# Kernel tuning notes

Measured on AMD Instinct MI355X. Metric: run time of the kernel, lower is better.

Reference implementation:

```python
import jax, jax.numpy as jnp
import numpy as np

EPS_NORM = 1e-12   # F.normalize eps
EPS_DIST = 1e-4    # sqrt stabilizer from original code
EPSILON = 1e-8     # log stabilizer (forward default arg)


def setup_inputs() -> dict:
    key = jax.random.key(0)
    thought_vectors = jax.random.normal(key, (4, 2048, 1024), dtype=jnp.float32)
    return {"thought_vectors": thought_vectors}


def reference(thought_vectors):
    # NOTE: original code casts to fp32 then discards it by re-reshaping the
    # raw input; inputs here are already fp32 so the math is identical.
    D = thought_vectors.shape[-1]
    x = thought_vectors.reshape(-1, D)                          # [N, D]
    norm = jnp.linalg.norm(x, axis=-1, keepdims=True)
    x = x / jnp.maximum(norm, EPS_NORM)                         # L2 normalize
    N = x.shape[0]
    sim = jnp.minimum(jnp.einsum('nd,md->nm', x, x), 1.0)       # [N, N], clamp max=1
    dists = jnp.sqrt(2.0 - 2.0 * sim + EPS_DIST)                # chordal distance
    dists = jnp.where(jnp.eye(N, dtype=bool), jnp.inf, dists)   # mask self
    min_dist = jnp.min(dists, axis=1)                           # nearest neighbor
    return -jnp.mean(jnp.log(min_dist + EPSILON))
```

## Files before the change

### kernel.cpp

```cpp
#include <hip/hip_runtime.h>
#include <hip/hip_bf16.h>
#include <math.h>

#define N_ROWS 8192
#define DIM    1024
#define NB     (N_ROWS / 128)
#define NT     (NB * (NB + 1) / 2)

typedef __bf16 bf16_t;
typedef __bf16 bf16x4 __attribute__((ext_vector_type(4)));
typedef __bf16 bf16x8 __attribute__((ext_vector_type(8)));
typedef float  f32x4  __attribute__((ext_vector_type(4)));

#define GLOAD_LDS(g, s) __builtin_amdgcn_global_load_lds(                      \
    (const __attribute__((address_space(1))) void*)(g),                        \
    (__attribute__((address_space(3))) void*)(s), 16, 0, 0)

__device__ __forceinline__ unsigned fmap(float f) {
    unsigned u = __float_as_uint(f);
    return (u & 0x80000000u) ? ~u : (u | 0x80000000u);
}
__device__ __forceinline__ float funmap(unsigned u) {
    return (u & 0x80000000u) ? __uint_as_float(u ^ 0x80000000u)
                             : __uint_as_float(~u);
}

__global__ __launch_bounds__(256) void k_normalize(const float* __restrict__ x,
                                                   bf16_t* __restrict__ xb,
                                                   unsigned* __restrict__ row_max) {
    const int row = blockIdx.x;
    const int tid = threadIdx.x;
    const float4* xr = reinterpret_cast<const float4*>(x + (size_t)row * DIM);
    float4 v = xr[tid];
    float ss = v.x * v.x + v.y * v.y + v.z * v.z + v.w * v.w;
    #pragma unroll
    for (int m = 32; m >= 1; m >>= 1) ss += __shfl_xor(ss, m);
    __shared__ float wss[4];
    if ((tid & 63) == 0) wss[tid >> 6] = ss;
    __syncthreads();
    const float tot = wss[0] + wss[1] + wss[2] + wss[3];
    const float scale = 1.0f / fmaxf(sqrtf(tot), 1e-12f);

    bf16x4 o;
    o[0] = (bf16_t)(v.x * scale);
    o[1] = (bf16_t)(v.y * scale);
    o[2] = (bf16_t)(v.z * scale);
    o[3] = (bf16_t)(v.w * scale);
    reinterpret_cast<bf16x4*>(xb + (size_t)row * DIM)[tid] = o;

    if (tid == 0) row_max[row] = 0u;
}

__global__ __launch_bounds__(256) void k_simmax(const bf16_t* __restrict__ xb,
                                                unsigned* __restrict__ row_max) {
    __shared__ bf16_t smA[128 * 32];
    __shared__ bf16_t smB[128 * 32];
    const int tid = threadIdx.x;
    const int w  = tid >> 6;
    const int l  = tid & 63;
    const int lr = l & 15;
    const int lk = (l >> 4) * 8;
    const int wr = w >> 1, wc = w & 1;

    int t = blockIdx.x;
    #define TOFF(b) ((b) * NB - ((b) * ((b) - 1)) / 2)
    int bi = (int)((float)(2 * NB + 1 -
                sqrtf((float)((2 * NB + 1) * (2 * NB + 1) - 8 * t))) * 0.5f);
    if (bi < 0) bi = 0;
    if (bi > NB - 1) bi = NB - 1;
    while (TOFF(bi + 1) <= t) ++bi;
    while (TOFF(bi) > t) --bi;
    const int bj = bi + (t - TOFF(bi));
    const int i0 = bi * 128, j0 = bj * 128;

    const bf16_t* gA = xb + (size_t)(i0 + (tid >> 2)) * DIM + (tid & 3) * 8;
    const bf16_t* gB = xb + (size_t)(j0 + (tid >> 2)) * DIM + (tid & 3) * 8;
    const int wbase = (tid & ~63) * 8;

    f32x4 acc[4][4] = {};
    const bf16_t* pa = smA + (wr * 64 + lr) * 32 + lk;
    const bf16_t* pb = smB + (wc * 64 + lr) * 32 + lk;

    for (int k = 0; k < DIM; k += 32) {
        GLOAD_LDS(gA + k,            smA + wbase);
        GLOAD_LDS(gA + 64 * DIM + k, smA + 2048 + wbase);
        GLOAD_LDS(gB + k,            smB + wbase);
        GLOAD_LDS(gB + 64 * DIM + k, smB + 2048 + wbase);
        __syncthreads();

        bf16x8 af[4], bf[4];
        #pragma unroll
        for (int m = 0; m < 4; ++m) af[m] = *(const bf16x8*)(pa + m * 512);
        #pragma unroll
        for (int n = 0; n < 4; ++n) bf[n] = *(const bf16x8*)(pb + n * 512);
        #pragma unroll
        for (int m = 0; m < 4; ++m)
            #pragma unroll
            for (int n = 0; n < 4; ++n)
                acc[m][n] = __builtin_amdgcn_mfma_f32_16x16x32_bf16(
                                af[m], bf[n], acc[m][n], 0, 0, 0);
        __syncthreads();
    }

    #pragma unroll
    for (int m = 0; m < 4; ++m) {
        #pragma unroll
        for (int j = 0; j < 4; ++j) {
            const int rowg = i0 + wr * 64 + m * 16 + (l >> 4) * 4 + j;
            float rm = -3.0e38f;
            #pragma unroll
            for (int n = 0; n < 4; ++n) {
                float s = acc[m][n][j];
                if (rowg == (j0 + wc * 64 + n * 16 + lr)) s = -3.0e38f;
                rm = fmaxf(rm, s);
            }
            #pragma unroll
            for (int mask = 1; mask < 16; mask <<= 1)
                rm = fmaxf(rm, __shfl_xor(rm, mask));
            if (lr == 0)
                atomicMax(&row_max[rowg], fmap(fminf(rm, 1.0f)));
        }
    }
    if (bi != bj) {
        #pragma unroll
        for (int n = 0; n < 4; ++n) {
            const int colg = j0 + wc * 64 + n * 16 + lr;
            float cm = -3.0e38f;
            #pragma unroll
            for (int m = 0; m < 4; ++m)
                #pragma unroll
                for (int j = 0; j < 4; ++j)
                    cm = fmaxf(cm, acc[m][n][j]);
            cm = fmaxf(cm, __shfl_xor(cm, 16));
            cm = fmaxf(cm, __shfl_xor(cm, 32));
            if (l < 16)
                atomicMax(&row_max[colg], fmap(fminf(cm, 1.0f)));
        }
    }
}

__global__ __launch_bounds__(256) void k_finish(const unsigned* __restrict__ row_max,
                                                float* __restrict__ out) {
    const int tid = threadIdx.x;
    float sum = 0.0f;
    for (int i = tid; i < N_ROWS; i += 256) {
        float sim = fminf(funmap(row_max[i]), 1.0f);
        float dist = sqrtf(2.0f - 2.0f * sim + 1e-4f);
        sum += logf(dist + 1e-8f);
    }
    #pragma unroll
    for (int m = 32; m >= 1; m >>= 1) sum += __shfl_xor(sum, m);
    __shared__ float wss[4];
    if ((tid & 63) == 0) wss[tid >> 6] = sum;
    __syncthreads();
    if (tid == 0) out[0] = -(wss[0] + wss[1] + wss[2] + wss[3]) / (float)N_ROWS;
}

extern "C" void kernel_launch(void* const* d_in, const int* in_sizes, int n_in,
                              void* d_out, int out_size, void* d_ws, size_t ws_size,
                              hipStream_t stream) {
    const float* x = (const float*)d_in[0];
    bf16_t* xb = (bf16_t*)d_ws;
    unsigned* row_max = (unsigned*)((char*)d_ws +
                         (size_t)N_ROWS * DIM * sizeof(bf16_t));
    float* out = (float*)d_out;

    k_normalize<<<N_ROWS, 256, 0, stream>>>(x, xb, row_max);
    k_simmax<<<NT, 256, 0, stream>>>(xb, row_max);
    k_finish<<<1, 256, 0, stream>>>(row_max, out);
}
```

Measured before the change: 186.4 us.

## Double-buffer LDS in simmax, one-wave-per-row normalize, wider finish reduction

The similarity GEMM kernel now uses two LDS buffers, so global-to-LDS loads for the next K step are issued before the MFMAs on the current step. This cuts one barrier per iteration and hides load latency. The normalize kernel now handles one row per wavefront with 4 rows per block, which removes the LDS reduction and block barrier, and it zeroes row_max with a strided pattern. The finish kernel moves to 1024 threads. Double buffering doubles LDS use per block, which may lower occupancy.

New measurement: 191.5 us. 1.03x slower.

```diff
diff --git a/kernel.cpp b/kernel.cpp
--- a/kernel.cpp
+++ b/kernel.cpp
@@ -28,33 +28,41 @@
 __global__ __launch_bounds__(256) void k_normalize(const float* __restrict__ x,
                                                    bf16_t* __restrict__ xb,
                                                    unsigned* __restrict__ row_max) {
-    const int row = blockIdx.x;
     const int tid = threadIdx.x;
+    const int l   = tid & 63;
+    const int row = blockIdx.x * 4 + (tid >> 6);
     const float4* xr = reinterpret_cast<const float4*>(x + (size_t)row * DIM);
-    float4 v = xr[tid];
-    float ss = v.x * v.x + v.y * v.y + v.z * v.z + v.w * v.w;
+
+    float4 v[4];
+    float ss = 0.0f;
+    #pragma unroll
+    for (int c = 0; c < 4; ++c) {
+        v[c] = xr[l + c * 64];
+        ss += v[c].x * v[c].x + v[c].y * v[c].y + v[c].z * v[c].z + v[c].w * v[c].w;
+    }
     #pragma unroll
     for (int m = 32; m >= 1; m >>= 1) ss += __shfl_xor(ss, m);
-    __shared__ float wss[4];
-    if ((tid & 63) == 0) wss[tid >> 6] = ss;
-    __syncthreads();
-    const float tot = wss[0] + wss[1] + wss[2] + wss[3];
-    const float scale = 1.0f / fmaxf(sqrtf(tot), 1e-12f);
-
-    bf16x4 o;
-    o[0] = (bf16_t)(v.x * scale);
-    o[1] = (bf16_t)(v.y * scale);
-    o[2] = (bf16_t)(v.z * scale);
-    o[3] = (bf16_t)(v.w * scale);
-    reinterpret_cast<bf16x4*>(xb + (size_t)row * DIM)[tid] = o;
-
-    if (tid == 0) row_max[row] = 0u;
+    const float scale = 1.0f / fmaxf(sqrtf(ss), 1e-12f);
+
+    bf16x4* xo = reinterpret_cast<bf16x4*>(xb + (size_t)row * DIM);
+    #pragma unroll
+    for (int c = 0; c < 4; ++c) {
+        bf16x4 o;
+        o[0] = (bf16_t)(v[c].x * scale);
+        o[1] = (bf16_t)(v[c].y * scale);
+        o[2] = (bf16_t)(v[c].z * scale);
+        o[3] = (bf16_t)(v[c].w * scale);
+        xo[l + c * 64] = o;
+    }
+
+    if (blockIdx.x < N_ROWS / 256)
+        row_max[blockIdx.x * 256 + tid] = 0u;
 }
 
 __global__ __launch_bounds__(256) void k_simmax(const bf16_t* __restrict__ xb,
                                                 unsigned* __restrict__ row_max) {
-    __shared__ bf16_t smA[128 * 32];
-    __shared__ bf16_t smB[128 * 32];
+    __shared__ bf16_t smA[2][128 * 32];
+    __shared__ bf16_t smB[2][128 * 32];
     const int tid = threadIdx.x;
     const int w  = tid >> 6;
     const int l  = tid & 63;
@@ -77,29 +85,48 @@
     const bf16_t* gB = xb + (size_t)(j0 + (tid >> 2)) * DIM + (tid & 3) * 8;
     const int wbase = (tid & ~63) * 8;
 
+    #define STAGE(buf, kk) do {                                                \
+        GLOAD_LDS(gA + (kk),            &smA[buf][wbase]);                     \
+        GLOAD_LDS(gA + 64 * DIM + (kk), &smA[buf][2048 + wbase]);              \
+        GLOAD_LDS(gB + (kk),            &smB[buf][wbase]);                     \
+        GLOAD_LDS(gB + 64 * DIM + (kk), &smB[buf][2048 + wbase]);              \
+    } while (0)
+
     f32x4 acc[4][4] = {};
-    const bf16_t* pa = smA + (wr * 64 + lr) * 32 + lk;
-    const bf16_t* pb = smB + (wc * 64 + lr) * 32 + lk;
-
-    for (int k = 0; k < DIM; k += 32) {
-        GLOAD_LDS(gA + k,            smA + wbase);
-        GLOAD_LDS(gA + 64 * DIM + k, smA + 2048 + wbase);
-        GLOAD_LDS(gB + k,            smB + wbase);
-        GLOAD_LDS(gB + 64 * DIM + k, smB + 2048 + wbase);
-        __syncthreads();
-
-        bf16x8 af[4], bf[4];
-        #pragma unroll
-        for (int m = 0; m < 4; ++m) af[m] = *(const bf16x8*)(pa + m * 512);
-        #pragma unroll
-        for (int n = 0; n < 4; ++n) bf[n] = *(const bf16x8*)(pb + n * 512);
+    const int fa = (wr * 64 + lr) * 32 + lk;
+    const int fb = (wc * 64 + lr) * 32 + lk;
+
+    STAGE(0, 0);
+    __syncthreads();
+    int cur = 0;
+    for (int k = 32; k < DIM; k += 32) {
+        STAGE(cur ^ 1, k);
+        bf16x8 af[4], bfr[4];
+        #pragma unroll
+        for (int m = 0; m < 4; ++m) af[m]  = *(const bf16x8*)(&smA[cur][fa + m * 512]);
+        #pragma unroll
+        for (int n = 0; n < 4; ++n) bfr[n] = *(const bf16x8*)(&smB[cur][fb + n * 512]);
         #pragma unroll
         for (int m = 0; m < 4; ++m)
             #pragma unroll
             for (int n = 0; n < 4; ++n)
                 acc[m][n] = __builtin_amdgcn_mfma_f32_16x16x32_bf16(
-                                af[m], bf[n], acc[m][n], 0, 0, 0);
+                                af[m], bfr[n], acc[m][n], 0, 0, 0);
         __syncthreads();
+        cur ^= 1;
+    }
+    {
+        bf16x8 af[4], bfr[4];
+        #pragma unroll
+        for (int m = 0; m < 4; ++m) af[m]  = *(const bf16x8*)(&smA[cur][fa + m * 512]);
+        #pragma unroll
+        for (int n = 0; n < 4; ++n) bfr[n] = *(const bf16x8*)(&smB[cur][fb + n * 512]);
+        #pragma unroll
+        for (int m = 0; m < 4; ++m)
+            #pragma unroll
+            for (int n = 0; n < 4; ++n)
+                acc[m][n] = __builtin_amdgcn_mfma_f32_16x16x32_bf16(
+                                af[m], bfr[n], acc[m][n], 0, 0, 0);
     }
 
     #pragma unroll
@@ -139,21 +166,27 @@
     }
 }
 
-__global__ __launch_bounds__(256) void k_finish(const unsigned* __restrict__ row_max,
-                                                float* __restrict__ out) {
+__global__ __launch_bounds__(1024) void k_finish(const unsigned* __restrict__ row_max,
+                                                 float* __restrict__ out) {
     const int tid = threadIdx.x;
     float sum = 0.0f;
-    for (int i = tid; i < N_ROWS; i += 256) {
+    #pragma unroll
+    for (int i = tid; i < N_ROWS; i += 1024) {
         float sim = fminf(funmap(row_max[i]), 1.0f);
         float dist = sqrtf(2.0f - 2.0f * sim + 1e-4f);
         sum += logf(dist + 1e-8f);
     }
     #pragma unroll
     for (int m = 32; m >= 1; m >>= 1) sum += __shfl_xor(sum, m);
-    __shared__ float wss[4];
+    __shared__ float wss[16];
     if ((tid & 63) == 0) wss[tid >> 6] = sum;
     __syncthreads();
-    if (tid == 0) out[0] = -(wss[0] + wss[1] + wss[2] + wss[3]) / (float)N_ROWS;
+    if (tid == 0) {
+        float tot = 0.0f;
+        #pragma unroll
+        for (int i = 0; i < 16; ++i) tot += wss[i];
+        out[0] = -tot / (float)N_ROWS;
+    }
 }
 
 extern "C" void kernel_launch(void* const* d_in, const int* in_sizes, int n_in,
@@ -165,7 +198,7 @@
                          (size_t)N_ROWS * DIM * sizeof(bf16_t));
     float* out = (float*)d_out;
 
-    k_normalize<<<N_ROWS, 256, 0, stream>>>(x, xb, row_max);
+    k_normalize<<<N_ROWS / 4, 256, 0, stream>>>(x, xb, row_max);
     k_simmax<<<NT, 256, 0, stream>>>(xb, row_max);
-    k_finish<<<1, 256, 0, stream>>>(row_max, out);
-}
+    k_finish<<<1, 1024, 0, stream>>>(row_max, out);
+}
```
